# Kernel optimization log

Measured on AMD Instinct MI355X. Metric: run time of the kernel, lower is better.

Reference implementation:

```python
import jax, jax.numpy as jnp
import numpy as np
from jax.scipy.special import gammaln

LENF = 15  # gamma unit-hydrograph length (UH_gamma default-ish routing window)
DT = 1.0


def setup_inputs() -> dict:
    key = jax.random.key(0)
    k = jax.random.split(key, 6)
    nb, nt, npar, nmul = 2000, 365, 12, 8
    return {
        "P": jax.random.uniform(k[0], (nb, nt), jnp.float32) * 10.0,   # precip mm/day
        "Ep": jax.random.uniform(k[1], (nb, nt), jnp.float32) * 5.0,   # PET mm/day
        "Tair": jax.random.normal(k[2], (nb, nt), jnp.float32) * 8.0,  # air temp C
        "params": jax.random.uniform(k[3], (nb, nt, npar, nmul), jnp.float32),  # raw [0,1]
        "rout_a": jax.random.uniform(k[4], (nb,), jnp.float32),
        "rout_b": jax.random.uniform(k[5], (nb,), jnp.float32),
    }


def reference(P, Ep, Tair, params, rout_a, rout_b):
    # P, Ep, Tair: [nb, nt]; params: [nb, nt, 12, nmul] raw in [0,1]
    nb, nt = P.shape
    nmul = params.shape[-1]
    dtype = P.dtype

    xs = (P.T, Ep.T, Tair.T, jnp.transpose(params, (1, 0, 2, 3)))  # time-major
    S0 = jnp.full((nb, nmul), 0.5, dtype)
    carry0 = (S0, S0, S0, S0, S0)  # snow, interception, soil, interflow, baseflow stores

    def step(carry, inp):
        S1, S2, S3, S4, S5 = carry
        Pt, Ept, Tt, pr = inp
        Pt, Ept, Tt = Pt[:, None], Ept[:, None], Tt[:, None]  # broadcast over nmul
        # parameter scaling (param_bounds: raw*(hi-lo)+lo), all [nb, nmul]
        tt    = -3.0 + pr[:, 0] * 8.0      # temp threshold
        ddf   = pr[:, 1] * 20.0            # degree-day melt factor
        Smax3 = 20.0 + pr[:, 3] * 680.0    # soil capacity
        p_lo  = 0.005 + pr[:, 4] * 0.99    # saturation_8 low frac
        p_hi  = 0.005 + pr[:, 5] * 0.99    # saturation_8 high frac
        p_exp = 1.0 + pr[:, 6] * 4.0       # recharge_2 exponent
        i1    = pr[:, 8]                   # interflow_4 linear coef
        i2    = pr[:, 9] * 1e-3            # interflow_4 quadratic coef
        kb    = pr[:, 10]                  # baseflow_1 coef

        # snowfall_1 / rainfall_1 via smoothThreshold_temperature_logistic (hard indicator)
        snowfrac = (Tt <= tt).astype(dtype)
        snow = Pt * snowfrac
        rain = Pt * (1.0 - snowfrac)
        # melt_1
        melt = jnp.clip(jnp.minimum(ddf * (Tt - tt), S1 / DT), 0.0)
        S1n = S1 + snow - melt
        # interception_1: In*(1 - smoothThreshold_storage_logistic)=In*0.95
        inter = rain * (1.0 - 0.05)
        # evap_1
        evap2 = jnp.minimum(S2 / DT, Ept)
        S2n = jnp.clip(S2 + (rain - inter) - evap2, 0.0)
        infil = melt + inter
        # saturation_8
        satexc = (p_lo + (p_hi - p_lo) * jnp.clip(S3, 0.0) / Smax3) * infil
        # effective_1
        rem = jnp.clip(infil - satexc, 0.0)
        # recharge_2
        rech = rem * (jnp.clip(S3, 0.0) / Smax3) ** p_exp
        # evap_7
        evap3 = jnp.minimum(jnp.clip(S3, 0.0) / Smax3 * Ept, S3 / DT)
        S3n = S3 + rem - rech - evap3
        # interflow_4
        S4c = jnp.clip(S4, 0.0)
        iflow = jnp.minimum(S4c, i1 * S4c + i2 * S4c ** 2)
        S4n = S4 + rech - iflow
        # baseflow_1
        base = kb * S5
        S5n = S5 + iflow - base
        Q = (satexc + base).mean(-1)  # average over nmul ensemble -> [nb]
        return (S1n, S2n, S3n, S4n, S5n), Q

    _, Q = jax.lax.scan(step, carry0, xs)  # Q: [nt, nb]
    Q = Q.T  # [nb, nt]

    # UH_gamma routing weights, normalized over lenF
    aa = jax.nn.relu(rout_a * 2.9) + 0.1   # [nb]
    th = jax.nn.relu(rout_b * 6.5) + 0.5
    t = jnp.arange(LENF, dtype=dtype)[:, None] + 0.5  # [lenF, 1], matches arange(0.5, lenF)
    denom = jnp.exp(gammaln(aa)) * th ** aa
    w = (1.0 / denom) * t ** (aa - 1.0) * jnp.exp(-t / th)  # [lenF, nb]
    w = w / w.sum(0)

    # UH_conv: grouped causal conv1d (flipped kernel, pad m-1, trim right)
    def causal_conv(q, wb):
        return jnp.convolve(q, wb, mode="full")[: q.shape[0]]

    Qrout = jax.vmap(causal_conv)(Q, w.T)  # [nb, nt]
    return Qrout
```

## Files before the change

kernel.cpp:

```cpp
#include <hip/hip_runtime.h>

#define NB      2000
#define NT      365
#define LENF    15
#define PSTRIDE 96

#define EXP2F(x) __builtin_amdgcn_exp2f(x)
#define LOG2F(x) __builtin_amdgcn_logf(x)
#define LOG2E    1.44269504088896f

template <int CTRL>
__device__ __forceinline__ float dpp_mov(float x) {
  int xi = __float_as_int(x);
  int r  = __builtin_amdgcn_update_dpp(xi, xi, CTRL, 0xF, 0xF, true);
  return __int_as_float(r);
}
#define DPP_XOR1   0xB1
#define DPP_XOR2   0x4E
#define DPP_HMIRR  0x141

__global__ __launch_bounds__(64) void prms_kernel(
    const float* __restrict__ P, const float* __restrict__ Ep,
    const float* __restrict__ Tair, const float* __restrict__ params,
    const float* __restrict__ rout_a, const float* __restrict__ rout_b,
    float* __restrict__ out)
{
  __shared__ float Qs[2][NT + 3];

  const int lane = threadIdx.x;
  const int m    = lane & 7;
  const int bsel = (lane >> 3) & 1;
  const int b0   = blockIdx.x * 2;
  const int b    = b0 + bsel;

  const float ra0 = rout_a[b0],     rb0 = rout_b[b0];
  const float ra1 = rout_a[b0 + 1], rb1 = rout_b[b0 + 1];

  const float* pl = params + (size_t)b * (NT * PSTRIDE) + m;
  const float* fP = P    + (size_t)b * NT;
  const float* fE = Ep   + (size_t)b * NT;
  const float* fT = Tair + (size_t)b * NT;

  float S1 = 0.5f, S2 = 0.5f, S3 = 0.5f, S4 = 0.5f, S5 = 0.5f;

  float rr[4][12];

  auto LOADP = [&](float* r, const float* lp, int so) {
    const float* q = lp + so * PSTRIDE;
    r[0] = q[0];   r[1] = q[8];   r[2] = q[24];
    r[3] = q[32];  r[4] = q[40];  r[5] = q[48];
    r[6] = q[64];  r[7] = q[72];  r[8] = q[80];
  };
  auto LOADF = [&](float* r, const float* p0, const float* p1, const float* p2, int o) {
    r[9]  = p0[o];
    r[10] = p1[o];
    r[11] = p2[o];
  };

  auto STEPD = [&](const float* d, int t) {
    const float tt    = fmaf(d[0], 8.0f, -3.0f);
    const float ddf   = d[1] * 20.0f;
    const float Smax3 = fmaf(d[2], 680.0f, 20.0f);
    const float p_lo  = fmaf(d[3], 0.99f, 0.005f);
    const float p_hi  = fmaf(d[4], 0.99f, 0.005f);
    const float p_exp = fmaf(d[5], 4.0f, 1.0f);
    const float i1    = d[6];
    const float i2    = d[7] * 0.001f;
    const float kb    = d[8];
    const float Pt    = d[9];
    const float Ept   = d[10];
    const float Tt    = d[11];

    const float snow = (Tt <= tt) ? Pt : 0.0f;
    const float rain = Pt - snow;
    const float melt = fmaxf(fminf(ddf * (Tt - tt), S1), 0.0f);
    S1 = S1 + snow - melt;

    const float inter = rain * 0.95f;
    const float evap2 = fminf(S2, Ept);
    S2 = fmaxf(S2 + (rain - inter) - evap2, 0.0f);

    const float infil  = melt + inter;
    const float frac   = fmaxf(S3, 0.0f) * __builtin_amdgcn_rcpf(Smax3);
    const float satexc = (p_lo + (p_hi - p_lo) * frac) * infil;
    const float rem    = fmaxf(infil - satexc, 0.0f);
    const float rech   = rem * EXP2F(p_exp * LOG2F(frac));
    const float evap3  = fminf(frac * Ept, S3);
    S3 = S3 + rem - rech - evap3;

    const float S4c   = fmaxf(S4, 0.0f);
    const float iflow = fminf(S4c, fmaf(i2, S4c * S4c, i1 * S4c));
    S4 = S4 + rech - iflow;

    const float base = kb * S5;
    S5 = S5 + iflow - base;

    float q = satexc + base;
    q += dpp_mov<DPP_XOR1>(q);
    q += dpp_mov<DPP_XOR2>(q);
    q += dpp_mov<DPP_HMIRR>(q);
    if ((lane & 55) == 0)
      Qs[bsel][t] = q * 0.125f;
  };

  #pragma unroll
  for (int s = 0; s < 4; ++s) {
    LOADP(rr[s], pl, s);
    LOADF(rr[s], fP, fE, fT, s);
  }

  const float* gp = pl;
  for (int g = 0; g < 45; ++g) {
    const int t0 = g * 8;
    const float* gp4 = gp + 4 * PSTRIDE;
    const float* gp8 = gp + 8 * PSTRIDE;
    #pragma unroll
    for (int s = 0; s < 8; ++s) {
      STEPD(rr[s & 3], t0 + s);
      if (s < 4) LOADP(rr[s & 3], gp4, s);
      else       LOADP(rr[s & 3], gp8, s - 4);
      LOADF(rr[s & 3], fP, fE, fT, s + 4);
    }
    gp += 8 * PSTRIDE; fP += 8; fE += 8; fT += 8;
  }
  {
    const float* gp4 = gp + 4 * PSTRIDE;
    #pragma unroll
    for (int s = 0; s < 5; ++s) {
      STEPD(rr[s & 3], 360 + s);
      if (s == 0) {
        LOADP(rr[0], gp4, 0);
        LOADF(rr[0], fP, fE, fT, 4);
      }
    }
  }

  __syncthreads();

  #pragma unroll
  for (int bs = 0; bs < 2; ++bs) {
    const float ra_v = bs ? ra1 : ra0;
    const float rb_v = bs ? rb1 : rb0;
    const float aa  = fmaxf(ra_v * 2.9f, 0.0f) + 0.1f;
    const float th  = fmaxf(rb_v * 6.5f, 0.0f) + 0.5f;
    const float am1 = aa - 1.0f;
    const float ith = -LOG2E / th;

    float w[LENF];
    float wsum = 0.0f;
    #pragma unroll
    for (int j = 0; j < LENF; ++j) {
      const float tj = (float)j + 0.5f;
      w[j] = EXP2F(fmaf(am1, LOG2F(tj), tj * ith));
      wsum += w[j];
    }
    const float inv = 1.0f / wsum;
    #pragma unroll
    for (int j = 0; j < LENF; ++j) w[j] *= inv;

    float* __restrict__ ob = out + (size_t)(b0 + bs) * NT;
    #pragma unroll
    for (int k = 0; k < 6; ++k) {
      const int t = lane + k * 64;
      if (t < NT) {
        float acc = 0.0f;
        #pragma unroll
        for (int j = 0; j < LENF; ++j) {
          const int idx = t - j;
          if (idx >= 0) acc += w[j] * Qs[bs][idx];
        }
        ob[t] = acc;
      }
    }
  }
}

extern "C" void kernel_launch(void* const* d_in, const int* in_sizes, int n_in,
                              void* d_out, int out_size, void* d_ws, size_t ws_size,
                              hipStream_t stream) {
  const float* P      = (const float*)d_in[0];
  const float* Ep     = (const float*)d_in[1];
  const float* Tair   = (const float*)d_in[2];
  const float* params = (const float*)d_in[3];
  const float* ra     = (const float*)d_in[4];
  const float* rb     = (const float*)d_in[5];
  float* out = (float*)d_out;

  prms_kernel<<<NB / 2, 64, 0, stream>>>(P, Ep, Tair, params, ra, rb, out);
}
```

Measured before the change: 92.30 us.

## Stage params and forcings into LDS via async global_load_lds double buffering

Replaces per-lane register prefetch of the strided params and forcing arrays with async global-to-LDS loads (global_load_lds) into a double-buffered shared tile of 8 timesteps. Each lane then reads its 12 values as three float4 LDS reads, packed contiguously per step. The aim is deeper memory latency hiding and fewer VGPRs spent on prefetch buffers. In exchange it adds LDS traffic, manual vmcnt/lgkmcnt waits and fragile index math for the address mapping.

```diff
diff --git a/kernel.cpp b/kernel.cpp
--- a/kernel.cpp
+++ b/kernel.cpp
@@ -1,13 +1,21 @@
 #include <hip/hip_runtime.h>
 
-#define NB      2000
-#define NT      365
-#define LENF    15
-#define PSTRIDE 96
+#define NB    2000
+#define NT    365
+#define LENF  15
+#define CH    8
+#define NCHF  45
+#define WPS   192
+#define WPC   (CH * WPS)
+#define BB    140160
 
 #define EXP2F(x) __builtin_amdgcn_exp2f(x)
 #define LOG2F(x) __builtin_amdgcn_logf(x)
 #define LOG2E    1.44269504088896f
+
+#define GLD4(g, l) __builtin_amdgcn_global_load_lds( \
+    (const __attribute__((address_space(1))) void*)(g), \
+    (__attribute__((address_space(3))) void*)(l), 4, 0, 0)
 
 template <int CTRL>
 __device__ __forceinline__ float dpp_mov(float x) {
@@ -25,51 +33,70 @@
     const float* __restrict__ rout_a, const float* __restrict__ rout_b,
     float* __restrict__ out)
 {
+  __shared__ __attribute__((aligned(16))) float sh[2][WPC];
   __shared__ float Qs[2][NT + 3];
 
   const int lane = threadIdx.x;
   const int m    = lane & 7;
   const int bsel = (lane >> 3) & 1;
   const int b0   = blockIdx.x * 2;
-  const int b    = b0 + bsel;
 
   const float ra0 = rout_a[b0],     rb0 = rout_b[b0];
   const float ra1 = rout_a[b0 + 1], rb1 = rout_b[b0 + 1];
 
-  const float* pl = params + (size_t)b * (NT * PSTRIDE) + m;
-  const float* fP = P    + (size_t)b * NT;
-  const float* fE = Ep   + (size_t)b * NT;
-  const float* fT = Tair + (size_t)b * NT;
+  const char* V0; const char* V1; const char* V2;
+  int St0, St1, St2;
+  {
+    const char* v[3]; int st[3];
+    #pragma unroll
+    for (int e = 0; e < 3; ++e) {
+      const int u   = e * 64 + lane;
+      const int r16 = (u * 171) >> 11;
+      const int k   = u - r16 * 12;
+      const int bs  = r16 >> 3;
+      const int mm  = r16 & 7;
+      if (k <= 8) {
+        const int pk = k + (k >= 2) + (k >= 6);
+        v[e]  = (const char*)params + (size_t)(b0 + bs) * BB + pk * 32 + mm * 4;
+        st[e] = 384;
+      } else {
+        const float* arr = (k == 9) ? P : (k == 10) ? Ep : Tair;
+        v[e]  = (const char*)(arr + (size_t)(b0 + bs) * NT);
+        st[e] = 4;
+      }
+    }
+    V0 = v[0]; V1 = v[1]; V2 = v[2];
+    St0 = st[0]; St1 = st[1]; St2 = st[2];
+  }
+
+  int tg = 0;
+  auto ISSUE = [&](int buf) {
+    #pragma unroll
+    for (int j = 0; j < CH; ++j) {
+      GLD4(V0, &sh[buf][j * WPS]);
+      GLD4(V1, &sh[buf][j * WPS + 64]);
+      GLD4(V2, &sh[buf][j * WPS + 128]);
+      if (tg < NT - 1) { V0 += St0; V1 += St1; V2 += St2; }
+      ++tg;
+    }
+  };
 
   float S1 = 0.5f, S2 = 0.5f, S3 = 0.5f, S4 = 0.5f, S5 = 0.5f;
-
-  float rr[4][12];
-
-  auto LOADP = [&](float* r, const float* lp, int so) {
-    const float* q = lp + so * PSTRIDE;
-    r[0] = q[0];   r[1] = q[8];   r[2] = q[24];
-    r[3] = q[32];  r[4] = q[40];  r[5] = q[48];
-    r[6] = q[64];  r[7] = q[72];  r[8] = q[80];
-  };
-  auto LOADF = [&](float* r, const float* p0, const float* p1, const float* p2, int o) {
-    r[9]  = p0[o];
-    r[10] = p1[o];
-    r[11] = p2[o];
-  };
-
-  auto STEPD = [&](const float* d, int t) {
-    const float tt    = fmaf(d[0], 8.0f, -3.0f);
-    const float ddf   = d[1] * 20.0f;
-    const float Smax3 = fmaf(d[2], 680.0f, 20.0f);
-    const float p_lo  = fmaf(d[3], 0.99f, 0.005f);
-    const float p_hi  = fmaf(d[4], 0.99f, 0.005f);
-    const float p_exp = fmaf(d[5], 4.0f, 1.0f);
-    const float i1    = d[6];
-    const float i2    = d[7] * 0.001f;
-    const float kb    = d[8];
-    const float Pt    = d[9];
-    const float Ept   = d[10];
-    const float Tt    = d[11];
+  const int rbase = (bsel * 8 + m) * 12;
+
+  auto STEPD = [&](float4 x0, float4 x1, float4 x2, int t) {
+    const float tt    = fmaf(x0.x, 8.0f, -3.0f);
+    const float ddf   = x0.y * 20.0f;
+    const float Smax3 = fmaf(x0.z, 680.0f, 20.0f);
+    const float p_lo  = fmaf(x0.w, 0.99f, 0.005f);
+    const float p_hi  = fmaf(x1.x, 0.99f, 0.005f);
+    const float p_exp = fmaf(x1.y, 4.0f, 1.0f);
+    const float i1    = x1.z;
+    const float i2    = x1.w * 0.001f;
+    const float kb    = x2.x;
+    const float Pt    = x2.y;
+    const float Ept   = x2.z;
+    const float Tt    = x2.w;
 
     const float snow = (Tt <= tt) ? Pt : 0.0f;
     const float rain = Pt - snow;
@@ -103,34 +130,41 @@
       Qs[bsel][t] = q * 0.125f;
   };
 
-  #pragma unroll
-  for (int s = 0; s < 4; ++s) {
-    LOADP(rr[s], pl, s);
-    LOADF(rr[s], fP, fE, fT, s);
-  }
-
-  const float* gp = pl;
-  for (int g = 0; g < 45; ++g) {
-    const int t0 = g * 8;
-    const float* gp4 = gp + 4 * PSTRIDE;
-    const float* gp8 = gp + 8 * PSTRIDE;
-    #pragma unroll
-    for (int s = 0; s < 8; ++s) {
-      STEPD(rr[s & 3], t0 + s);
-      if (s < 4) LOADP(rr[s & 3], gp4, s);
-      else       LOADP(rr[s & 3], gp8, s - 4);
-      LOADF(rr[s & 3], fP, fE, fT, s + 4);
-    }
-    gp += 8 * PSTRIDE; fP += 8; fE += 8; fT += 8;
-  }
+  ISSUE(0);
+  ISSUE(1);
+  for (int c = 0; c < NCHF; ++c) {
+    asm volatile("s_waitcnt vmcnt(24)" ::: "memory");
+    const int buf = c & 1;
+    const int t0  = c * CH;
+    const float4* rp = (const float4*)&sh[buf][rbase];
+    float4 a0, a1, a2, c0, c1, c2;
+    a0 = rp[0]; a1 = rp[1]; a2 = rp[2];
+    #pragma unroll
+    for (int s = 0; s < CH; ++s) {
+      if ((s & 1) == 0) {
+        if (s < CH - 1) { c0 = rp[(s+1)*48]; c1 = rp[(s+1)*48+1]; c2 = rp[(s+1)*48+2]; }
+        STEPD(a0, a1, a2, t0 + s);
+      } else {
+        if (s < CH - 1) { a0 = rp[(s+1)*48]; a1 = rp[(s+1)*48+1]; a2 = rp[(s+1)*48+2]; }
+        STEPD(c0, c1, c2, t0 + s);
+      }
+    }
+    asm volatile("s_waitcnt lgkmcnt(0)" ::: "memory");
+    if (c <= NCHF - 2) ISSUE(buf);
+  }
+  asm volatile("s_waitcnt vmcnt(0)" ::: "memory");
   {
-    const float* gp4 = gp + 4 * PSTRIDE;
+    const float4* rp = (const float4*)&sh[1][rbase];
+    float4 a0, a1, a2, c0, c1, c2;
+    a0 = rp[0]; a1 = rp[1]; a2 = rp[2];
     #pragma unroll
     for (int s = 0; s < 5; ++s) {
-      STEPD(rr[s & 3], 360 + s);
-      if (s == 0) {
-        LOADP(rr[0], gp4, 0);
-        LOADF(rr[0], fP, fE, fT, 4);
+      if ((s & 1) == 0) {
+        if (s < 4) { c0 = rp[(s+1)*48]; c1 = rp[(s+1)*48+1]; c2 = rp[(s+1)*48+2]; }
+        STEPD(a0, a1, a2, 360 + s);
+      } else {
+        if (s < 4) { a0 = rp[(s+1)*48]; a1 = rp[(s+1)*48+1]; a2 = rp[(s+1)*48+2]; }
+        STEPD(c0, c1, c2, 360 + s);
       }
     }
   }
```

After: 105.9 us. 1.15x slower.
